# Kernel tuning notes

Measured on AMD Instinct MI355X. Metric: run time of the kernel, lower is better.

The kernel has to match this reference:

```python
import jax, jax.numpy as jnp
import numpy as np
from functools import partial

IMG = 608
H = W = 76            # grid size (stride 8 head)
A = 3                 # anchors per scale
C = 80                # classes
BA = 5 + C            # bbox attrs
STRIDE = IMG / float(H)
ANCHORS = np.array([[10., 13.], [16., 30.], [33., 23.]], dtype=np.float32)
SC_ANCH = ANCHORS / STRIDE          # anchors in grid units
IGNORE_THR = 0.5
OBJ_SCALE = 1.0
NOOBJ_SCALE = 100.0


def setup_inputs() -> dict:
    key = jax.random.key(0)
    k1, k2, k3, k4 = jax.random.split(key, 4)
    B, T = 16, 50
    pred = jax.random.normal(k1, (B, A * BA, H, W), dtype=jnp.float32)
    xy = jax.random.uniform(k2, (B, T, 2), minval=0.01, maxval=0.99, dtype=jnp.float32)
    wh = jax.random.uniform(k3, (B, T, 2), minval=0.02, maxval=0.30, dtype=jnp.float32)
    cls_id = jax.random.randint(k4, (B, T, 1), 0, C).astype(jnp.float32)
    targets = jnp.concatenate([xy, wh, cls_id], axis=-1)  # [B, T, 5] normalized
    return {"pred": pred, "targets": targets}


def build_targets(targets):
    """Faithful vectorized+scan version of YOlOLoss.build_targets."""
    B, T, _ = targets.shape
    mult = jnp.array([W, H, W, H, 1.0], dtype=jnp.float32)
    tb = targets * mult                      # scale x,w by W and y,h by H; class untouched
    gx, gy, gw, gh, gc = (tb[..., i] for i in range(5))
    valid = (gx + gy + gw + gh) != 0.0       # torch: skip rows whose first 4 entries sum to 0
    gi = jnp.floor(gx).astype(jnp.int32)
    gj = jnp.floor(gy).astype(jnp.int32)
    gi = jnp.where(gi == 0, 1, gi)           # quirk in original: 0 -> 1
    gj = jnp.where(gj == 0, 1, gj)

    aw = jnp.asarray(SC_ANCH[:, 0])          # [A]
    ah = jnp.asarray(SC_ANCH[:, 1])
    # IoU of corner-aligned boxes [0,0,w,h]
    inter = jnp.minimum(gw[..., None], aw) * jnp.minimum(gh[..., None], ah)   # [B,T,A]
    union = gw[..., None] * gh[..., None] + 1e-16 + aw * ah - inter
    ious = inter / union
    best = jnp.argmax(ious, axis=-1).astype(jnp.int32)                        # [B,T]
    ign = ious > IGNORE_THR                                                   # [B,T,A]

    bidx = jnp.broadcast_to(jnp.arange(B, dtype=jnp.int32)[:, None], (B, T))
    flat = lambda a: a.reshape((B * T,) + a.shape[2:])
    xs = {"b": flat(bidx), "v": flat(valid), "gi": flat(gi), "gj": flat(gj),
          "n": flat(best), "ign": flat(ign), "gx": flat(gx), "gy": flat(gy),
          "gw": flat(gw), "gh": flat(gh), "cls": flat(gc).astype(jnp.int32)}

    z = jnp.zeros((B, A, H, W), jnp.float32)
    init = (jnp.zeros((B, A, H, W), bool),          # obj_mask
            jnp.ones((B, A, H, W), bool),           # noobj_mask
            z, z, z, z, z,                          # tx, ty, tw, th, tconf
            jnp.zeros((B, A, H, W, C), jnp.float32))  # tcls

    def step(carry, s):
        obj, noobj, tx, ty, tw, th, tconf, tcls = carry
        b, v, gi, gj, n = s["b"], s["v"], s["gi"], s["gj"], s["n"]
        # ignore-anchor suppression; NOTE original indexes (gi, gj) here (swapped quirk)
        cur = noobj[b, :, gi, gj]
        noobj = noobj.at[b, :, gi, gj].set(jnp.where(v & s["ign"], False, cur))

        def upd(arr, idx, val):
            return arr.at[idx].set(jnp.where(v, val, arr[idx]))

        obj = upd(obj, (b, n, gj, gi), True)
        noobj = upd(noobj, (b, n, gj, gi), False)
        tx = upd(tx, (b, n, gj, gi), s["gx"] - gi.astype(jnp.float32))
        ty = upd(ty, (b, n, gj, gi), s["gy"] - gj.astype(jnp.float32))
        tw = upd(tw, (b, n, gj, gi), jnp.log(s["gw"] / aw[n] + 1e-16))
        th = upd(th, (b, n, gj, gi), jnp.log(s["gh"] / ah[n] + 1e-16))
        tconf = upd(tconf, (b, n, gj, gi), 1.0)
        tcls = upd(tcls, (b, n, gj, gi, s["cls"]), 1.0)
        return (obj, noobj, tx, ty, tw, th, tconf, tcls), None

    carry, _ = jax.lax.scan(step, init, xs)
    return carry


def _masked_mse(p, t, m, n):
    return jnp.sum(m * (p - t) ** 2) / n


def _masked_bce(p, t, m, n):
    # torch BCELoss clamps log terms at -100
    lp = jnp.maximum(jnp.log(p), -100.0)
    l1p = jnp.maximum(jnp.log1p(-p), -100.0)
    return jnp.sum(m * (-(t * lp + (1.0 - t) * l1p))) / n


def yolo_loss(pred, tgt_grids):
    B = pred.shape[0]
    obj, noobj, tx, ty, tw, th, tconf, tcls = tgt_grids
    p = pred.reshape(B, A, BA, H, W).transpose(0, 1, 3, 4, 2)   # [B,A,H,W,5+C]
    x = jax.nn.sigmoid(p[..., 0])
    y = jax.nn.sigmoid(p[..., 1])
    w_ = p[..., 2]
    h_ = p[..., 3]
    conf = jax.nn.sigmoid(p[..., 4])
    pcls = jax.nn.sigmoid(p[..., 5:])

    of = obj.astype(jnp.float32)
    nf = noobj.astype(jnp.float32)
    n_obj = jnp.maximum(jnp.sum(of), 1.0)
    n_noobj = jnp.maximum(jnp.sum(nf), 1.0)

    loss_x = _masked_mse(x, tx, of, n_obj)
    loss_y = _masked_mse(y, ty, of, n_obj)
    loss_w = _masked_mse(w_, tw, of, n_obj)
    loss_h = _masked_mse(h_, th, of, n_obj)
    loss_conf_obj = _masked_bce(conf, tconf, of, n_obj)
    loss_conf_noobj = _masked_bce(conf, tconf, nf, n_noobj)
    loss_conf = OBJ_SCALE * loss_conf_obj + NOOBJ_SCALE * loss_conf_noobj
    loss_cls = _masked_bce(pcls, tcls, of[..., None], n_obj * C)
    return loss_x + loss_y + loss_w + loss_h + loss_conf + loss_cls


@jax.jit
def _run(pred, targets):
    return yolo_loss(pred, build_targets(targets))


def reference(pred, targets):
    return _run(pred, targets)
```

## Files before the change

kernel.cpp:

```cpp
#include <hip/hip_runtime.h>
#include <math.h>

#define BB 16
#define TT 50
#define AA 3
#define CC 80
#define BA_ 85
#define HH 76
#define WW 76
#define SPAT (HH * WW)
#define NPLANE (BB * AA)
#define NQ (SPAT / 4)
#define P4 (BA_ * NQ)
#define TOTAL4 (NPLANE * P4)
#define GRID 2048
#define NTH 256

__constant__ float c_aw[3] = {1.25f, 2.0f, 4.125f};
__constant__ float c_ah[3] = {1.625f, 3.75f, 2.875f};

struct Rec { float tx, ty, tw, th; unsigned m0, m1, m2, pad; };

__device__ inline float wave_red(float v) {
    #pragma unroll
    for (int off = 32; off; off >>= 1) v += __shfl_down(v, off);
    return v;
}

__global__ __launch_bounds__(256) void k_build(const float* __restrict__ targets,
                                               unsigned char* __restrict__ state,
                                               Rec* __restrict__ recs) {
    const int b = blockIdx.x;
    const int tid = threadIdx.x;
    __shared__ int sh_valid[TT], sh_best[TT], sh_mcell[TT], sh_cls[TT];

    int4* pl = (int4*)(state + (size_t)b * AA * SPAT);
    for (int k = tid; k < (AA * SPAT) / 16; k += 256) pl[k] = make_int4(0, 0, 0, 0);

    int valid = 0, best = 0, mcell = 0, icell = 0, ign = 0;
    float txv = 0.f, tyv = 0.f, twv = 0.f, thv = 0.f;
    if (tid < TT) {
        const float* tg = targets + ((size_t)b * TT + tid) * 5;
        float gx = tg[0] * WW, gy = tg[1] * HH;
        float gw = tg[2] * WW, gh = tg[3] * HH;
        int cls = (int)tg[4];
        valid = (gx + gy + gw + gh != 0.0f) ? 1 : 0;
        int gi = (int)floorf(gx); if (gi == 0) gi = 1;
        int gj = (int)floorf(gy); if (gj == 0) gj = 1;
        float bi = -1.f;
        #pragma unroll
        for (int a = 0; a < 3; ++a) {
            float inter = fminf(gw, c_aw[a]) * fminf(gh, c_ah[a]);
            float uni = gw * gh + 1e-16f + c_aw[a] * c_ah[a] - inter;
            float iou = inter / uni;
            if (iou > bi) { bi = iou; best = a; }
            if (iou > 0.5f) ign |= 1 << a;
        }
        icell = gi * WW + gj;
        mcell = gj * WW + gi;
        txv = gx - (float)gi;
        tyv = gy - (float)gj;
        twv = logf(gw / c_aw[best] + 1e-16f);
        thv = logf(gh / c_ah[best] + 1e-16f);
        sh_valid[tid] = valid; sh_best[tid] = best;
        sh_mcell[tid] = mcell; sh_cls[tid] = cls;
    }
    __syncthreads();

    unsigned char* st = state + (size_t)b * AA * SPAT;
    if (tid < TT && valid) {
        #pragma unroll
        for (int a = 0; a < 3; ++a)
            if ((ign >> a) & 1) st[a * SPAT + icell] = 1;
        st[best * SPAT + mcell] = 1;
    }
    __syncthreads();

    if (tid < TT && valid) {
        bool owner = true;
        for (int t2 = tid + 1; t2 < TT; ++t2)
            if (sh_valid[t2] && sh_mcell[t2] == mcell && sh_best[t2] == best) {
                owner = false; break;
            }
        if (owner) {
            unsigned m0 = 0u, m1 = 0u, m2 = 0u;
            for (int t2 = 0; t2 < TT; ++t2)
                if (sh_valid[t2] && sh_mcell[t2] == mcell && sh_best[t2] == best) {
                    int c = sh_cls[t2];
                    if (c < 32) m0 |= 1u << c;
                    else if (c < 64) m1 |= 1u << (c - 32);
                    else m2 |= 1u << (c - 64);
                }
            Rec r; r.tx = txv; r.ty = tyv; r.tw = twv; r.th = thv;
            r.m0 = m0; r.m1 = m1; r.m2 = m2; r.pad = 0u;
            recs[b * TT + tid] = r;
            st[best * SPAT + mcell] = (unsigned char)(2 + tid);
        }
    }
}

__global__ __launch_bounds__(256) void k_dense(const float* __restrict__ pred,
                                               const unsigned char* __restrict__ state,
                                               const Rec* __restrict__ recs,
                                               float* __restrict__ part) {
    const int tid = blockIdx.x * NTH + threadIdx.x;
    float s_mse = 0.f, s_bo = 0.f, s_bn = 0.f, s_bc = 0.f, s_no = 0.f, s_cn = 0.f;

    for (int f = tid; f < TOTAL4; f += GRID * NTH) {
        float4 z4 = *reinterpret_cast<const float4*>(pred + (size_t)f * 4);
        asm volatile("" :: "v"(z4.x), "v"(z4.y), "v"(z4.z), "v"(z4.w));

        int p = f / P4;
        int r = f - p * P4;
        int c = r / NQ;
        int s0 = (r - c * NQ) * 4;
        uchar4 s4 = *reinterpret_cast<const uchar4*>(state + (size_t)p * SPAT + s0);
        int st[4] = {s4.x, s4.y, s4.z, s4.w};
        float zz[4] = {z4.x, z4.y, z4.z, z4.w};
        int b = p / AA;

        if (c == 4) {
            #pragma unroll
            for (int k = 0; k < 4; ++k) {
                float conf = 1.f / (1.f + expf(-zz[k]));
                if (st[k] == 0) {
                    s_cn += 1.f;
                    s_bn += -fmaxf(log1pf(-conf), -100.f);
                } else if (st[k] >= 2) {
                    s_bo += -fmaxf(logf(conf), -100.f);
                }
            }
        } else if (c < 4) {
            #pragma unroll
            for (int k = 0; k < 4; ++k)
                if (st[k] >= 2) {
                    const Rec rr = recs[b * TT + st[k] - 2];
                    float tv = (c == 0) ? rr.tx : (c == 1) ? rr.ty
                             : (c == 2) ? rr.tw : rr.th;
                    float v = (c < 2) ? 1.f / (1.f + expf(-zz[k])) : zz[k];
                    s_mse += (v - tv) * (v - tv);
                    if (c == 0) s_no += 1.f;
                }
        } else {
            int ci = c - 5;
            #pragma unroll
            for (int k = 0; k < 4; ++k)
                if (st[k] >= 2) {
                    const Rec rr = recs[b * TT + st[k] - 2];
                    unsigned wd = (ci < 32) ? rr.m0 : (ci < 64) ? rr.m1 : rr.m2;
                    int tcv = (wd >> (ci & 31)) & 1;
                    float pr = 1.f / (1.f + expf(-zz[k]));
                    s_bc += tcv ? -fmaxf(logf(pr), -100.f)
                                : -fmaxf(log1pf(-pr), -100.f);
                }
        }
    }

    s_mse = wave_red(s_mse); s_bo = wave_red(s_bo); s_bn = wave_red(s_bn);
    s_bc  = wave_red(s_bc);  s_no = wave_red(s_no); s_cn = wave_red(s_cn);
    __shared__ float red[4][6];
    int wv = threadIdx.x >> 6, ln = threadIdx.x & 63;
    if (ln == 0) {
        red[wv][0] = s_mse; red[wv][1] = s_bo; red[wv][2] = s_bn;
        red[wv][3] = s_bc;  red[wv][4] = s_no; red[wv][5] = s_cn;
    }
    __syncthreads();
    if (threadIdx.x == 0) {
        #pragma unroll
        for (int k = 0; k < 6; ++k)
            part[blockIdx.x * 6 + k] =
                red[0][k] + red[1][k] + red[2][k] + red[3][k];
    }
}

__global__ __launch_bounds__(256) void k_final(const float* __restrict__ part,
                                               float* __restrict__ out) {
    const int tid = threadIdx.x;
    float v[6] = {0.f, 0.f, 0.f, 0.f, 0.f, 0.f};
    for (int i = tid; i < GRID; i += 256) {
        #pragma unroll
        for (int k = 0; k < 6; ++k) v[k] += part[i * 6 + k];
    }
    #pragma unroll
    for (int k = 0; k < 6; ++k) v[k] = wave_red(v[k]);
    __shared__ float red[4][6];
    int wv = tid >> 6, ln = tid & 63;
    if (ln == 0) {
        #pragma unroll
        for (int k = 0; k < 6; ++k) red[wv][k] = v[k];
    }
    __syncthreads();
    if (tid == 0) {
        float m[6];
        #pragma unroll
        for (int k = 0; k < 6; ++k)
            m[k] = red[0][k] + red[1][k] + red[2][k] + red[3][k];
        float n_obj   = fmaxf(m[4], 1.f);
        float n_noobj = fmaxf(m[5], 1.f);
        out[0] = m[0] / n_obj
               + m[1] / n_obj
               + 100.f * (m[2] / n_noobj)
               + m[3] / (n_obj * (float)CC);
    }
}

extern "C" void kernel_launch(void* const* d_in, const int* in_sizes, int n_in,
                              void* d_out, int out_size, void* d_ws, size_t ws_size,
                              hipStream_t stream) {
    const float* pred    = (const float*)d_in[0];
    const float* targets = (const float*)d_in[1];
    float* out = (float*)d_out;
    char* ws = (char*)d_ws;

    Rec*           recs  = (Rec*)ws;
    unsigned char* state = (unsigned char*)(ws + 25600);
    float*         part  = (float*)(ws + 302848);

    k_build<<<BB, 256, 0, stream>>>(targets, state, recs);
    k_dense<<<GRID, NTH, 0, stream>>>(pred, state, recs, part);
    k_final<<<1, 256, 0, stream>>>(part, out);
}
```

Before: 161.3 us.

## Read only confidence plane densely and gather object cells sparsely

The dense sweep over all 85 channels of the prediction tensor is replaced by a sweep of only the confidence channel for the no-object term. A separate group of blocks, one wave per target record, gathers the 85 channel values at each owning cell for the coordinate, objectness and class losses. Because nearly every cell is no-object, most of the tensor never contributed anything, so this cuts memory traffic by roughly the channel count. The cost is strided single-element gathers for object cells and a record layout that now stores a precomputed base offset.

New measurement: 139.5 us. 1.16x faster.

```diff
diff --git a/kernel.cpp b/kernel.cpp
--- a/kernel.cpp
+++ b/kernel.cpp
@@ -9,17 +9,16 @@
 #define HH 76
 #define WW 76
 #define SPAT (HH * WW)
-#define NPLANE (BB * AA)
 #define NQ (SPAT / 4)
-#define P4 (BA_ * NQ)
-#define TOTAL4 (NPLANE * P4)
-#define GRID 2048
-#define NTH 256
+#define NCONF4 (BB * AA * NQ)
+#define NCONFB ((NCONF4 + 255) / 256)
+#define NOBJB (BB * TT / 4)
+#define GRID2 (NCONFB + NOBJB)
 
 __constant__ float c_aw[3] = {1.25f, 2.0f, 4.125f};
 __constant__ float c_ah[3] = {1.625f, 3.75f, 2.875f};
 
-struct Rec { float tx, ty, tw, th; unsigned m0, m1, m2, pad; };
+struct Rec { int base; float tx, ty, tw, th; unsigned m0, m1, m2; };
 
 __device__ inline float wave_red(float v) {
     #pragma unroll
@@ -74,102 +73,117 @@
             if ((ign >> a) & 1) st[a * SPAT + icell] = 1;
         st[best * SPAT + mcell] = 1;
     }
-    __syncthreads();
-
-    if (tid < TT && valid) {
-        bool owner = true;
-        for (int t2 = tid + 1; t2 < TT; ++t2)
-            if (sh_valid[t2] && sh_mcell[t2] == mcell && sh_best[t2] == best) {
-                owner = false; break;
+
+    if (tid < TT) {
+        Rec r; r.base = -1;
+        r.tx = txv; r.ty = tyv; r.tw = twv; r.th = thv;
+        r.m0 = 0u; r.m1 = 0u; r.m2 = 0u;
+        if (valid) {
+            bool owner = true;
+            for (int t2 = tid + 1; t2 < TT; ++t2)
+                if (sh_valid[t2] && sh_mcell[t2] == mcell && sh_best[t2] == best) {
+                    owner = false; break;
+                }
+            if (owner) {
+                unsigned m0 = 0u, m1 = 0u, m2 = 0u;
+                for (int t2 = 0; t2 < TT; ++t2)
+                    if (sh_valid[t2] && sh_mcell[t2] == mcell && sh_best[t2] == best) {
+                        int c = sh_cls[t2];
+                        if (c < 32) m0 |= 1u << c;
+                        else if (c < 64) m1 |= 1u << (c - 32);
+                        else m2 |= 1u << (c - 64);
+                    }
+                r.base = ((b * AA + best) * BA_) * SPAT + mcell;
+                r.m0 = m0; r.m1 = m1; r.m2 = m2;
             }
-        if (owner) {
-            unsigned m0 = 0u, m1 = 0u, m2 = 0u;
-            for (int t2 = 0; t2 < TT; ++t2)
-                if (sh_valid[t2] && sh_mcell[t2] == mcell && sh_best[t2] == best) {
-                    int c = sh_cls[t2];
-                    if (c < 32) m0 |= 1u << c;
-                    else if (c < 64) m1 |= 1u << (c - 32);
-                    else m2 |= 1u << (c - 64);
-                }
-            Rec r; r.tx = txv; r.ty = tyv; r.tw = twv; r.th = thv;
-            r.m0 = m0; r.m1 = m1; r.m2 = m2; r.pad = 0u;
-            recs[b * TT + tid] = r;
-            st[best * SPAT + mcell] = (unsigned char)(2 + tid);
-        }
-    }
-}
-
-__global__ __launch_bounds__(256) void k_dense(const float* __restrict__ pred,
+        }
+        recs[b * TT + tid] = r;
+    }
+}
+
+__global__ __launch_bounds__(256) void k_sweep(const float* __restrict__ pred,
                                                const unsigned char* __restrict__ state,
                                                const Rec* __restrict__ recs,
                                                float* __restrict__ part) {
-    const int tid = blockIdx.x * NTH + threadIdx.x;
+    const int blk = blockIdx.x;
+    const int tid = threadIdx.x;
     float s_mse = 0.f, s_bo = 0.f, s_bn = 0.f, s_bc = 0.f, s_no = 0.f, s_cn = 0.f;
 
-    for (int f = tid; f < TOTAL4; f += GRID * NTH) {
-        float4 z4 = *reinterpret_cast<const float4*>(pred + (size_t)f * 4);
-        asm volatile("" :: "v"(z4.x), "v"(z4.y), "v"(z4.z), "v"(z4.w));
-
-        int p = f / P4;
-        int r = f - p * P4;
-        int c = r / NQ;
-        int s0 = (r - c * NQ) * 4;
-        uchar4 s4 = *reinterpret_cast<const uchar4*>(state + (size_t)p * SPAT + s0);
-        int st[4] = {s4.x, s4.y, s4.z, s4.w};
-        float zz[4] = {z4.x, z4.y, z4.z, z4.w};
-        int b = p / AA;
-
-        if (c == 4) {
+    if (blk < NCONFB) {
+        int f = blk * 256 + tid;
+        if (f < NCONF4) {
+            int p = f / NQ;
+            int q = f - p * NQ;
+            float4 z4 = *reinterpret_cast<const float4*>(
+                pred + ((size_t)p * BA_ + 4) * SPAT + q * 4);
+            uchar4 s4 = *reinterpret_cast<const uchar4*>(
+                state + (size_t)p * SPAT + q * 4);
+            int st[4] = {s4.x, s4.y, s4.z, s4.w};
+            float zz[4] = {z4.x, z4.y, z4.z, z4.w};
             #pragma unroll
-            for (int k = 0; k < 4; ++k) {
-                float conf = 1.f / (1.f + expf(-zz[k]));
+            for (int k = 0; k < 4; ++k)
                 if (st[k] == 0) {
+                    float conf = 1.f / (1.f + expf(-zz[k]));
                     s_cn += 1.f;
                     s_bn += -fmaxf(log1pf(-conf), -100.f);
-                } else if (st[k] >= 2) {
-                    s_bo += -fmaxf(logf(conf), -100.f);
                 }
+        }
+    } else {
+        int r = (blk - NCONFB) * 4 + (tid >> 6);
+        int lane = tid & 63;
+        Rec rr = recs[r];
+        if (rr.base >= 0) {
+            float z  = pred[(size_t)rr.base + (size_t)lane * SPAT];
+            float z2 = 0.f;
+            if (lane < BA_ - 64)
+                z2 = pred[(size_t)rr.base + (size_t)(64 + lane) * SPAT];
+
+            if (lane == 0) {
+                float x = 1.f / (1.f + expf(-z));
+                s_mse += (x - rr.tx) * (x - rr.tx);
+                s_no += 1.f;
+            } else if (lane == 1) {
+                float y = 1.f / (1.f + expf(-z));
+                s_mse += (y - rr.ty) * (y - rr.ty);
+            } else if (lane == 2) {
+                s_mse += (z - rr.tw) * (z - rr.tw);
+            } else if (lane == 3) {
+                s_mse += (z - rr.th) * (z - rr.th);
+            } else if (lane == 4) {
+                float cf = 1.f / (1.f + expf(-z));
+                s_bo += -fmaxf(logf(cf), -100.f);
+            } else {
+                int ci = lane - 5;
+                unsigned wd = (ci < 32) ? rr.m0 : rr.m1;
+                int tcv = (wd >> (ci & 31)) & 1;
+                float p = 1.f / (1.f + expf(-z));
+                s_bc += tcv ? -fmaxf(logf(p), -100.f)
+                            : -fmaxf(log1pf(-p), -100.f);
             }
-        } else if (c < 4) {
-            #pragma unroll
-            for (int k = 0; k < 4; ++k)
-                if (st[k] >= 2) {
-                    const Rec rr = recs[b * TT + st[k] - 2];
-                    float tv = (c == 0) ? rr.tx : (c == 1) ? rr.ty
-                             : (c == 2) ? rr.tw : rr.th;
-                    float v = (c < 2) ? 1.f / (1.f + expf(-zz[k])) : zz[k];
-                    s_mse += (v - tv) * (v - tv);
-                    if (c == 0) s_no += 1.f;
-                }
-        } else {
-            int ci = c - 5;
-            #pragma unroll
-            for (int k = 0; k < 4; ++k)
-                if (st[k] >= 2) {
-                    const Rec rr = recs[b * TT + st[k] - 2];
-                    unsigned wd = (ci < 32) ? rr.m0 : (ci < 64) ? rr.m1 : rr.m2;
-                    int tcv = (wd >> (ci & 31)) & 1;
-                    float pr = 1.f / (1.f + expf(-zz[k]));
-                    s_bc += tcv ? -fmaxf(logf(pr), -100.f)
-                                : -fmaxf(log1pf(-pr), -100.f);
-                }
+            if (lane < BA_ - 64) {
+                int ci = 59 + lane;
+                unsigned wd = (ci < 64) ? rr.m1 : rr.m2;
+                int tcv = (wd >> (ci & 31)) & 1;
+                float p = 1.f / (1.f + expf(-z2));
+                s_bc += tcv ? -fmaxf(logf(p), -100.f)
+                            : -fmaxf(log1pf(-p), -100.f);
+            }
         }
     }
 
     s_mse = wave_red(s_mse); s_bo = wave_red(s_bo); s_bn = wave_red(s_bn);
     s_bc  = wave_red(s_bc);  s_no = wave_red(s_no); s_cn = wave_red(s_cn);
     __shared__ float red[4][6];
-    int wv = threadIdx.x >> 6, ln = threadIdx.x & 63;
+    int wv = tid >> 6, ln = tid & 63;
     if (ln == 0) {
         red[wv][0] = s_mse; red[wv][1] = s_bo; red[wv][2] = s_bn;
         red[wv][3] = s_bc;  red[wv][4] = s_no; red[wv][5] = s_cn;
     }
     __syncthreads();
-    if (threadIdx.x == 0) {
+    if (tid == 0) {
         #pragma unroll
         for (int k = 0; k < 6; ++k)
-            part[blockIdx.x * 6 + k] =
-                red[0][k] + red[1][k] + red[2][k] + red[3][k];
+            part[blk * 6 + k] = red[0][k] + red[1][k] + red[2][k] + red[3][k];
     }
 }
 
@@ -177,7 +191,7 @@
                                                float* __restrict__ out) {
     const int tid = threadIdx.x;
     float v[6] = {0.f, 0.f, 0.f, 0.f, 0.f, 0.f};
-    for (int i = tid; i < GRID; i += 256) {
+    for (int i = tid; i < GRID2; i += 256) {
         #pragma unroll
         for (int k = 0; k < 6; ++k) v[k] += part[i * 6 + k];
     }
@@ -217,6 +231,6 @@
     float*         part  = (float*)(ws + 302848);
 
     k_build<<<BB, 256, 0, stream>>>(targets, state, recs);
-    k_dense<<<GRID, NTH, 0, stream>>>(pred, state, recs, part);
+    k_sweep<<<GRID2, 256, 0, stream>>>(pred, state, recs, part);
     k_final<<<1, 256, 0, stream>>>(part, out);
 }
```
